# Kernel tuning notes

Hardware: AMD Instinct MI355X
Metric: run time of the kernel (lower is better)

## Reference

```python
import jax, jax.numpy as jnp
import numpy as np

DIM = 96; HEADS = 3; DHEAD = 32; GSS = 4; PATCH = 32; B = 128; G = 8
INNER = HEADS * DHEAD  # == DIM
SCALE = DHEAD ** -0.5
EPS = 1e-5


def _rbf(x):
    # FastKAN RBF basis on grid [-2, 2] with G centers -> (..., G)
    centers = jnp.linspace(-2.0, 2.0, G)
    h = 4.0 / (G - 1)
    return jnp.exp(-(((x[..., None] - centers) / h) ** 2))


def _kan_pointwise(x, wb, ws):
    # Pointwise KAN conv: (b, Cin, *spatial) -> (b, Cout, *spatial)
    # y = W_base @ silu(x) + W_spline @ rbf(x)
    b, cin = x.shape[0], x.shape[1]
    sp = x.shape[2:]
    xs = x.reshape(b, cin, -1)                       # (b, Cin, L)
    y = jnp.einsum('oi,bil->bol', wb, jax.nn.silu(xs))
    y = y + jnp.einsum('oig,bilg->bol', ws, _rbf(xs))
    return y.reshape(b, wb.shape[0], *sp)


def setup_inputs() -> dict:
    key = jax.random.key(0)
    ks = jax.random.split(key, 8)
    inp = {
        'x': jax.random.normal(ks[0], (B, DIM, PATCH, PATCH), jnp.float32),
        'group_tokens': jax.random.normal(ks[1], (DIM,), jnp.float32),
        'qkv_wb': jax.random.normal(ks[2], (3 * DIM, DIM), jnp.float32) * (DIM ** -0.5),
        'qkv_ws': jax.random.normal(ks[3], (3 * DIM, DIM, G), jnp.float32) * 0.02,
        'ln_g': jnp.ones((DHEAD,), jnp.float32),
        'ln_b': jnp.zeros((DHEAD,), jnp.float32),
        'gt_wb': jax.random.normal(ks[4], (2 * INNER, INNER), jnp.float32) * (INNER ** -0.5),
        'gt_ws': jax.random.normal(ks[5], (2 * INNER, INNER, G), jnp.float32) * 0.02,
        'out_wb': jax.random.normal(ks[6], (DIM, INNER), jnp.float32) * (INNER ** -0.5),
        'out_ws': jax.random.normal(ks[7], (DIM, INNER, G), jnp.float32) * 0.02,
    }
    return inp


def reference(x, group_tokens, qkv_wb, qkv_ws, ln_g, ln_b, gt_wb, gt_ws, out_wb, out_ws):
    b, c, H, W = x.shape
    g = GSS
    nx, ny = H // g, W // g
    nw = nx * ny                                    # number of windows
    bp = b * nw
    n = g * g + 1                                   # window tokens incl. group token

    # b c (h g1) (w g2) -> (b h w) c (g1 g2)
    xw = x.reshape(b, c, nx, g, ny, g).transpose(0, 2, 4, 1, 3, 5).reshape(bp, c, g * g)
    tok = jnp.broadcast_to(group_tokens[None, :, None], (bp, c, 1))
    xw = jnp.concatenate([tok, xw], axis=-1)        # (bp, c, n)

    qkv = _kan_pointwise(xw, qkv_wb, qkv_ws)        # (bp, 3c, n)
    q, k, v = jnp.split(qkv, 3, axis=1)

    def split_heads(t):  # b (h d) n -> b h n d
        return t.reshape(bp, HEADS, DHEAD, n).transpose(0, 1, 3, 2)

    q, k, v = map(split_heads, (q, k, v))
    q = q * SCALE
    # channel-attention within window: contract over token axis n
    dots = jnp.einsum('bhni,bhnj->bhij', q, k)      # (bp, h, d, d)
    attn = jax.nn.softmax(dots, axis=-1)
    out = jnp.einsum('bhij,bhnj->bhni', attn, v)    # (bp, h, n, d)

    gt = out[:, :, 0]                               # (bp, h, d) group tokens
    gf = out[:, :, 1:]                              # (bp, h, g*g, d)
    gt = gt.reshape(b, nw, HEADS, DHEAD).transpose(0, 2, 1, 3)            # (b, h, nw, d)
    gf = gf.reshape(b, nw, HEADS, g * g, DHEAD).transpose(0, 2, 1, 3, 4)  # (b, h, nw, gg, d)

    # group_tokens_to_qk: LN(d) -> GELU -> KAN conv over nw (channels h*d -> 2*h*d)
    mu = gt.mean(-1, keepdims=True)
    var = ((gt - mu) ** 2).mean(-1, keepdims=True)
    h_ = (gt - mu) * jax.lax.rsqrt(var + EPS) * ln_g + ln_b
    h_ = jax.nn.gelu(h_, approximate=False)
    hh = h_.transpose(0, 1, 3, 2).reshape(b, HEADS * DHEAD, nw)           # b (h c) n
    qk = _kan_pointwise(hh, gt_wb, gt_ws)                                 # (b, 2*h*d, nw)
    qk = qk.reshape(b, HEADS, 2 * DHEAD, nw).transpose(0, 1, 3, 2)        # (b, h, nw, 2d)
    w_q, w_k = jnp.split(qk, 2, axis=-1)
    w_q = w_q * SCALE
    w_attn = jax.nn.softmax(jnp.einsum('bhid,bhjd->bhij', w_q, w_k), axis=-1)
    agg = jnp.einsum('bhij,bhjwd->bhiwd', w_attn, gf)                     # (b, h, nw, gg, d)

    # b h (x y) (g1 g2) d -> b (h d) (x g1) (y g2)
    fmap = agg.reshape(b, HEADS, nx, ny, g, g, DHEAD)
    fmap = fmap.transpose(0, 1, 6, 2, 4, 3, 5).reshape(b, HEADS * DHEAD, H, W)

    return _kan_pointwise(fmap, out_wb, out_ws)     # (b, dim, H, W)
```

## Files before the change

### kernel.cpp

```cpp
#include <hip/hip_runtime.h>
#include <cstddef>

#define SCALE 0.17677669529663687f
#define EPS 1e-5f

typedef __attribute__((ext_vector_type(8))) __bf16 bf16x8;
typedef __attribute__((ext_vector_type(16))) float f32x16;
typedef __attribute__((ext_vector_type(8))) unsigned short ushort8;

__device__ __forceinline__ unsigned short f2bf(float f) {
    unsigned u = __float_as_uint(f);
    return (unsigned short)((u + 0x7fffu + ((u >> 16) & 1u)) >> 16);
}
__device__ __forceinline__ float bf2f(unsigned short h) {
    return __uint_as_float(((unsigned)h) << 16);
}
__device__ __forceinline__ unsigned cvt_pk_bf16(float a, float b) {
    unsigned r;
    asm("v_cvt_pk_bf16_f32 %0, %1, %2" : "=v"(r) : "v"(a), "v"(b));
    return r;
}

#define MFMA32(a, b, c) __builtin_amdgcn_mfma_f32_32x32x16_bf16(a, b, c, 0, 0, 0)

#define GLD_LDS16(gsrc, ldst) \
    __builtin_amdgcn_global_load_lds((const __attribute__((address_space(1))) void*)(gsrc), \
                                     (__attribute__((address_space(3))) void*)(ldst), 16, 0, 0)

__global__ __launch_bounds__(256)
void prep_frag32(const float* __restrict__ wb, const float* __restrict__ ws,
                 unsigned short* __restrict__ Wf, int MTT)
{
    int idx = blockIdx.x * 256 + threadIdx.x;
    int total = 27 * MTT * 4 * 64;
    if (idx >= total) return;
    int lane = idx & 63;
    int t = idx >> 6;
    int hl = t & 1, kf = (t >> 1) & 1;
    int mt = (t >> 2) % MTT, s = (t >> 2) / MTT;
    int cg = s / 9, f = s - cg * 9;
    int m = mt * 32 + (lane & 31);
    int kg = lane >> 5;
    ushort8 v;
    #pragma unroll
    for (int j = 0; j < 8; ++j) {
        int c = cg * 32 + kf * 16 + kg * 8 + j;
        float w = (f == 0) ? wb[m * 96 + c] : ws[(m * 96 + c) * 8 + (f - 1)];
        unsigned short hi = f2bf(w);
        v[j] = hl ? f2bf(w - bf2f(hi)) : hi;
    }
    *reinterpret_cast<ushort8*>(Wf + (size_t)t * 512 + lane * 8) = v;
}

template<int MTT, int MODE>
__global__ __launch_bounds__(256, 2)
void kan_mfma(const float* __restrict__ xin, const float* __restrict__ token,
              const unsigned short* __restrict__ Wf, float* __restrict__ out)
{
    __shared__ __align__(16) char smem[2 * 12 * 1024];

    const int tid = threadIdx.x, lane = tid & 63, wid = tid >> 6;
    const int kg = lane >> 5, cl = lane & 31;

    int n0, mb;
    if (MODE == 0) {
        int xcd = blockIdx.x & 7, idx = blockIdx.x >> 3;
        int nloc = idx / 3; mb = idx - nloc * 3;
        n0 = (xcd * 68 + nloc) * 256;
    } else {
        mb = blockIdx.x & 1; n0 = (blockIdx.x >> 1) * 256;
    }

    auto issueA = [&](int s, int buf) {
        #pragma unroll
        for (int c0 = 0; c0 < 3; ++c0) {
            int c = wid + c0 * 4;
            const unsigned short* src = Wf + ((size_t)s * MTT * 4 + mb * 12 + c) * 512 + lane * 8;
            GLD_LDS16(src, smem + (buf * 12 + c) * 1024);
        }
    };
    issueA(0, 0);

    const float* gbv[2];
    int gsv[2];
    #pragma unroll
    for (int nt = 0; nt < 2; ++nt) {
        int p = n0 + wid * 64 + nt * 32 + cl;
        if (MODE == 0) {
            int w = p / 17, l = p - w * 17;
            if (l == 0) { gbv[nt] = token; gsv[nt] = 1; }
            else {
                int b = w >> 6, wl = w & 63;
                int wx = wl >> 3, wy = wl & 7;
                int jj = l - 1, gx = jj >> 2, gy = jj & 3;
                gbv[nt] = xin + (size_t)b * 98304 + (wx * 4 + gx) * 32 + wy * 4 + gy;
                gsv[nt] = 1024;
            }
        } else {
            gbv[nt] = xin + (size_t)(p >> 6) * 6144 + (p & 63);
            gsv[nt] = 64;
        }
    }

    f32x16 acc[2][3];
    #pragma unroll
    for (int nt = 0; nt < 2; ++nt)
        #pragma unroll
        for (int mt = 0; mt < 3; ++mt)
            #pragma unroll
            for (int r = 0; r < 16; ++r) acc[nt][mt][r] = 0.f;

    float rr[2][16], du[2][16];
    bf16x8 pk[2][2];

    auto phiInit = [&](int cg) {
        #pragma unroll
        for (int nt = 0; nt < 2; ++nt) {
            float ph[16];
            #pragma unroll
            for (int t = 0; t < 2; ++t)
                #pragma unroll
                for (int j = 0; j < 8; ++j) {
                    int q = t * 8 + j;
                    float xv = gbv[nt][(size_t)(cg * 32 + t * 16 + kg * 8 + j) * gsv[nt]];
                    ph[q] = __fdividef(xv, 1.f + __expf(-xv));
                    float a = fmaf(xv, 1.75f, 3.5f);
                    rr[nt][q] = __expf(-a * a);
                    du[nt][q] = __expf(fminf(fmaf(a, 2.f, -1.f), 80.f));
                }
            #pragma unroll
            for (int t = 0; t < 2; ++t) {
                uint4 w;
                w.x = cvt_pk_bf16(ph[t * 8 + 0], ph[t * 8 + 1]);
                w.y = cvt_pk_bf16(ph[t * 8 + 2], ph[t * 8 + 3]);
                w.z = cvt_pk_bf16(ph[t * 8 + 4], ph[t * 8 + 5]);
                w.w = cvt_pk_bf16(ph[t * 8 + 6], ph[t * 8 + 7]);
                pk[nt][t] = *reinterpret_cast<bf16x8*>(&w);
            }
        }
    };
    auto phiRbf = [&](bool upd) {
        #pragma unroll
        for (int nt = 0; nt < 2; ++nt) {
            if (upd) {
                #pragma unroll
                for (int q = 0; q < 16; ++q) { rr[nt][q] *= du[nt][q]; du[nt][q] *= 0.1353352832366127f; }
            }
            #pragma unroll
            for (int t = 0; t < 2; ++t) {
                uint4 w;
                w.x = cvt_pk_bf16(rr[nt][t * 8 + 0], rr[nt][t * 8 + 1]);
                w.y = cvt_pk_bf16(rr[nt][t * 8 + 2], rr[nt][t * 8 + 3]);
                w.z = cvt_pk_bf16(rr[nt][t * 8 + 4], rr[nt][t * 8 + 5]);
                w.w = cvt_pk_bf16(rr[nt][t * 8 + 6], rr[nt][t * 8 + 7]);
                pk[nt][t] = *reinterpret_cast<bf16x8*>(&w);
            }
        }
    };

    #pragma unroll
    for (int s = 0; s < 27; ++s) {
        __syncthreads();
        if (s + 1 < 27) issueA(s + 1, (s + 1) & 1);
        const int fn = s % 9;
        if (fn == 0) phiInit(s / 9);
        else phiRbf(fn != 1);

        const char* Ab = smem + (s & 1) * 12288;
        #pragma unroll
        for (int mt = 0; mt < 3; ++mt) {
            const char* fb = Ab + mt * 4096 + lane * 16;
            bf16x8 b0h = *reinterpret_cast<const bf16x8*>(fb);
            bf16x8 b0l = *reinterpret_cast<const bf16x8*>(fb + 1024);
            bf16x8 b1h = *reinterpret_cast<const bf16x8*>(fb + 2048);
            bf16x8 b1l = *reinterpret_cast<const bf16x8*>(fb + 3072);
            #pragma unroll
            for (int nt = 0; nt < 2; ++nt) {
                acc[nt][mt] = MFMA32(pk[nt][0], b0h, acc[nt][mt]);
                acc[nt][mt] = MFMA32(pk[nt][0], b0l, acc[nt][mt]);
                acc[nt][mt] = MFMA32(pk[nt][1], b1h, acc[nt][mt]);
                acc[nt][mt] = MFMA32(pk[nt][1], b1l, acc[nt][mt]);
            }
        }
    }

    if (MODE == 0) {
        #pragma unroll
        for (int nt = 0; nt < 2; ++nt)
            #pragma unroll
            for (int r = 0; r < 16; ++r) {
                int p = n0 + wid * 64 + nt * 32 + (r & 3) + 8 * (r >> 2) + 4 * kg;
                int w = p / 17, l = p - w * 17;
                float* dst = out + (size_t)w * 4896 + l * 288 + mb * 96 + cl;
                dst[0]  = acc[nt][0][r];
                dst[32] = acc[nt][1][r];
                dst[64] = acc[nt][2][r];
            }
    } else {
        #pragma unroll
        for (int nt = 0; nt < 2; ++nt)
            #pragma unroll
            for (int r = 0; r < 16; ++r) {
                int p = n0 + wid * 64 + nt * 32 + (r & 3) + 8 * (r >> 2) + 4 * kg;
                float* dst = out + (size_t)p * 192 + mb * 96 + cl;
                dst[0]  = acc[nt][0][r];
                dst[32] = acc[nt][1][r];
                dst[64] = acc[nt][2][r];
            }
    }
}

__global__ __launch_bounds__(256, 4)
void kan_mfma_fmap(const float* __restrict__ xin,
                   const unsigned short* __restrict__ Wf, float* __restrict__ out)
{
    __shared__ __align__(16) char smem[40960];
    char* sA = smem;
    char* sB = smem + 24576;

    const int tid = threadIdx.x, lane = tid & 63, wid = tid >> 6;

    int xcd = blockIdx.x & 7;
    int n0 = (xcd * 128 + (blockIdx.x >> 3)) * 128;

    auto issueA = [&](int s, int buf) {
        #pragma unroll
        for (int c0 = 0; c0 < 3; ++c0) {
            int c = wid + c0 * 4;
            const unsigned short* src = Wf + ((size_t)s * 12 + c) * 512 + lane * 8;
            GLD_LDS16(src, sA + (buf * 12 + c) * 1024);
        }
    };
    issueA(0, 0);

    const int ct = tid & 127, kgp = tid >> 7;
    const int lane_in = kgp * 32 + (ct & 31);
    const int p = n0 + ct;
    const float* gbase = xin + (size_t)(p >> 10) * 98304 + (p & 1023);

    f32x16 acc[3];
    #pragma unroll
    for (int mt = 0; mt < 3; ++mt)
        #pragma unroll
        for (int r = 0; r < 16; ++r) acc[mt][r] = 0.f;

    float rr[16], du[16];

    auto phiInit = [&](int cg, char* d0, char* d1) {
        float ph[16];
        #pragma unroll
        for (int t = 0; t < 2; ++t)
            #pragma unroll
            for (int j = 0; j < 8; ++j) {
                int q = t * 8 + j;
                float xv = gbase[(size_t)(cg * 32 + t * 16 + kgp * 8 + j) * 1024];
                ph[q] = __fdividef(xv, 1.f + __expf(-xv));
                float a = fmaf(xv, 1.75f, 3.5f);
                rr[q] = __expf(-a * a);
                du[q] = __expf(fminf(fmaf(a, 2.f, -1.f), 80.f));
            }
        uint4 w0, w1;
        w0.x = cvt_pk_bf16(ph[0], ph[1]);  w0.y = cvt_pk_bf16(ph[2], ph[3]);
        w0.z = cvt_pk_bf16(ph[4], ph[5]);  w0.w = cvt_pk_bf16(ph[6], ph[7]);
        w1.x = cvt_pk_bf16(ph[8], ph[9]);  w1.y = cvt_pk_bf16(ph[10], ph[11]);
        w1.z = cvt_pk_bf16(ph[12], ph[13]); w1.w = cvt_pk_bf16(ph[14], ph[15]);
        *reinterpret_cast<uint4*>(d0) = w0;
        *reinterpret_cast<uint4*>(d1) = w1;
    };
    auto phiRbf = [&](bool upd, char* d0, char* d1) {
        if (upd) {
            #pragma unroll
            for (int q = 0; q < 16; ++q) { rr[q] *= du[q]; du[q] *= 0.1353352832366127f; }
        }
        uint4 w0, w1;
        w0.x = cvt_pk_bf16(rr[0], rr[1]);  w0.y = cvt_pk_bf16(rr[2], rr[3]);
        w0.z = cvt_pk_bf16(rr[4], rr[5]);  w0.w = cvt_pk_bf16(rr[6], rr[7]);
        w1.x = cvt_pk_bf16(rr[8], rr[9]);  w1.y = cvt_pk_bf16(rr[10], rr[11]);
        w1.z = cvt_pk_bf16(rr[12], rr[13]); w1.w = cvt_pk_bf16(rr[14], rr[15]);
        *reinterpret_cast<uint4*>(d0) = w0;
        *reinterpret_cast<uint4*>(d1) = w1;
    };

    phiInit(0, sB + (ct >> 5) * 1024 + lane_in * 16,
               sB + (4 + (ct >> 5)) * 1024 + lane_in * 16);

    #pragma unroll
    for (int s = 0; s < 27; ++s) {
        int sb = s & 1;
        __syncthreads();
        if (s + 1 < 27) issueA(s + 1, (s + 1) & 1);
        {
            const char* Ab = sA + sb * 12288;
            const char* Bb = sB + sb * 8192;
            bf16x8 b0 = *reinterpret_cast<const bf16x8*>(Bb + wid * 1024 + lane * 16);
            bf16x8 b1 = *reinterpret_cast<const bf16x8*>(Bb + (4 + wid) * 1024 + lane * 16);
            #pragma unroll
            for (int mt = 0; mt < 3; ++mt) {
                const char* fb = Ab + mt * 4096 + lane * 16;
                bf16x8 a0 = *reinterpret_cast<const bf16x8*>(fb);
                bf16x8 a1 = *reinterpret_cast<const bf16x8*>(fb + 1024);
                bf16x8 a2 = *reinterpret_cast<const bf16x8*>(fb + 2048);
                bf16x8 a3 = *reinterpret_cast<const bf16x8*>(fb + 3072);
                acc[mt] = MFMA32(a0, b0, acc[mt]);
                acc[mt] = MFMA32(a1, b0, acc[mt]);
                acc[mt] = MFMA32(a2, b1, acc[mt]);
                acc[mt] = MFMA32(a3, b1, acc[mt]);
            }
        }
        if (s + 1 < 27) {
            char* d0 = sB + ((s + 1) & 1) * 8192 + (ct >> 5) * 1024 + lane_in * 16;
            int fn = (s + 1) % 9;
            if (fn == 0) phiInit((s + 1) / 9, d0, d0 + 4096);
            else phiRbf(fn != 1, d0, d0 + 4096);
        }
    }

    const int colL = n0 + wid * 32 + (lane & 31);
    #pragma unroll
    for (int mt = 0; mt < 3; ++mt) {
        #pragma unroll
        for (int r = 0; r < 16; ++r) {
            int row = mt * 32 + (r & 3) + 8 * (r >> 2) + 4 * (lane >> 5);
            out[(size_t)(colL >> 10) * 98304 + (size_t)row * 1024 + (colL & 1023)] = acc[mt][r];
        }
    }
}

__global__ __launch_bounds__(256)
void attn1(const float* __restrict__ qkv, float* __restrict__ gt, float* __restrict__ gf)
{
    __shared__ float sw[17][288];
    __shared__ float sa[3][32][33];
    const int w = blockIdx.x, tid = threadIdx.x;

    const float4* src = reinterpret_cast<const float4*>(qkv + (size_t)w * 4896);
    float4* dstl = reinterpret_cast<float4*>(&sw[0][0]);
    for (int e = tid; e < 1224; e += 256) dstl[e] = src[e];
    __syncthreads();

    for (int e = tid; e < 3072; e += 256) {
        int h = e >> 10, r = e & 1023, i = r >> 5, j = r & 31;
        float s = 0.f;
        #pragma unroll
        for (int l = 0; l < 17; ++l) s += sw[l][h * 32 + i] * sw[l][96 + h * 32 + j];
        sa[h][i][j] = s * SCALE;
    }
    __syncthreads();
    if (tid < 96) {
        int h = tid >> 5, i = tid & 31;
        float m = -1e30f;
        for (int j = 0; j < 32; ++j) m = fmaxf(m, sa[h][i][j]);
        float sum = 0.f;
        for (int j = 0; j < 32; ++j) { float e_ = __expf(sa[h][i][j] - m); sa[h][i][j] = e_; sum += e_; }
        float inv = 1.f / sum;
        for (int j = 0; j < 32; ++j) sa[h][i][j] *= inv;
    }
    __syncthreads();
    const int b = w >> 6, wl = w & 63;
    for (int e = tid; e < 1632; e += 256) {
        int h = e / 544, r = e - h * 544, l = r >> 5, i = r & 31;
        float s = 0.f;
        #pragma unroll
        for (int j = 0; j < 32; ++j) s += sa[h][i][j] * sw[l][192 + h * 32 + j];
        if (l == 0) gt[(((size_t)b * 3 + h) * 64 + wl) * 32 + i] = s;
        else        gf[((((size_t)b * 3 + h) * 64 + wl) * 16 + (l - 1)) * 32 + i] = s;
    }
}

__global__ __launch_bounds__(256)
void ln_gelu(const float* __restrict__ gt, const float* __restrict__ lng,
             const float* __restrict__ lnb, float* __restrict__ hh)
{
    int row = blockIdx.x * 8 + (threadIdx.x >> 5);
    int d = threadIdx.x & 31;
    float x = gt[(size_t)row * 32 + d];
    float s = x, s2 = x * x;
    #pragma unroll
    for (int m = 16; m >= 1; m >>= 1) { s += __shfl_xor(s, m, 32); s2 += __shfl_xor(s2, m, 32); }
    float mu = s * (1.f / 32.f);
    float var = s2 * (1.f / 32.f) - mu * mu;
    float h = (x - mu) * rsqrtf(var + EPS) * lng[d] + lnb[d];
    float g = 0.5f * h * (1.f + erff(h * 0.70710678118654752f));
    int b = row / 192, r = row - b * 192;
    int hd = r >> 6, wl = r & 63;
    hh[((size_t)b * 96 + hd * 32 + d) * 64 + wl] = g;
}

__global__ __launch_bounds__(256)
void attn2a(const float* __restrict__ qk, float* __restrict__ wattn)
{
    int bh = blockIdx.x;
    int b = bh / 3, h = bh - b * 3;
    __shared__ float swq[64][33];
    __shared__ float swk[64][33];
    __shared__ float sd[64][65];
    int tid = threadIdx.x;
    for (int e = tid; e < 2048; e += 256) {
        int i = e >> 5, d = e & 31;
        const float* row = qk + ((size_t)b * 64 + i) * 192 + h * 64;
        swq[i][d] = row[d] * SCALE;
        swk[i][d] = row[32 + d];
    }
    __syncthreads();
    for (int e = tid; e < 4096; e += 256) {
        int i = e >> 6, j = e & 63;
        float s = 0.f;
        #pragma unroll
        for (int d = 0; d < 32; ++d) s += swq[i][d] * swk[j][d];
        sd[i][j] = s;
    }
    __syncthreads();
    if (tid < 64) {
        float m = -1e30f;
        for (int j = 0; j < 64; ++j) m = fmaxf(m, sd[tid][j]);
        float sum = 0.f;
        for (int j = 0; j < 64; ++j) { float e_ = __expf(sd[tid][j] - m); sd[tid][j] = e_; sum += e_; }
        float inv = 1.f / sum;
        for (int j = 0; j < 64; ++j) sd[tid][j] *= inv;
    }
    __syncthreads();
    for (int e = tid; e < 4096; e += 256)
        wattn[(size_t)bh * 4096 + e] = sd[e >> 6][e & 63];
}

__global__ __launch_bounds__(256)
void attn2b(const float* __restrict__ wattn, const float* __restrict__ gf,
            float* __restrict__ fmap)
{
    int blk = blockIdx.x;
    int ct = blk & 3, bh = blk >> 2;
    int b = bh / 3, h = bh - b * 3;
    __shared__ float sa[64][65];
    __shared__ float sg[64][129];
    int tid = threadIdx.x;
    for (int e = tid; e < 4096; e += 256) sa[e >> 6][e & 63] = wattn[(size_t)bh * 4096 + e];
    for (int e = tid; e < 8192; e += 256) {
        int j = e >> 7, c = e & 127;
        sg[j][c] = gf[((size_t)bh * 64 + j) * 512 + ct * 128 + c];
    }
    __syncthreads();
    int txc = tid & 31, tyi = tid >> 5;
    float acc[8][4];
    #pragma unroll
    for (int ii = 0; ii < 8; ++ii)
        #pragma unroll
        for (int c = 0; c < 4; ++c) acc[ii][c] = 0.f;
    for (int j = 0; j < 64; ++j) {
        float g0[4];
        #pragma unroll
        for (int c = 0; c < 4; ++c) g0[c] = sg[j][txc + c * 32];
        #pragma unroll
        for (int ii = 0; ii < 8; ++ii) {
            float a = sa[tyi + ii * 8][j];
            #pragma unroll
            for (int c = 0; c < 4; ++c) acc[ii][c] += a * g0[c];
        }
    }
    __syncthreads();
    #pragma unroll
    for (int ii = 0; ii < 8; ++ii)
        #pragma unroll
        for (int c = 0; c < 4; ++c)
            sg[tyi + ii * 8][txc + c * 32] = acc[ii][c];
    __syncthreads();
    for (int e = tid; e < 8192; e += 256) {
        int d = e >> 8;
        int nx = (e >> 5) & 7;
        int cp = e & 31;
        int ny = cp >> 2, gy = cp & 3;
        float v = sg[nx * 8 + ny][gy * 32 + d];
        fmap[(((size_t)b * 96 + h * 32 + d) * 32 + nx * 4 + ct) * 32 + cp] = v;
    }
}

extern "C" void kernel_launch(void* const* d_in, const int* in_sizes, int n_in,
                              void* d_out, int out_size, void* d_ws, size_t ws_size,
                              hipStream_t stream)
{
    const float* x      = (const float*)d_in[0];
    const float* tok    = (const float*)d_in[1];
    const float* qkv_wb = (const float*)d_in[2];
    const float* qkv_ws = (const float*)d_in[3];
    const float* lng    = (const float*)d_in[4];
    const float* lnb    = (const float*)d_in[5];
    const float* gt_wb  = (const float*)d_in[6];
    const float* gt_ws  = (const float*)d_in[7];
    const float* out_wb = (const float*)d_in[8];
    const float* out_ws = (const float*)d_in[9];
    float* out = (float*)d_out;
    float* ws  = (float*)d_ws;

    const size_t OFF_QKV   = 0;
    const size_t OFF_FMAP  = 0;
    const size_t OFF_WATTN = 12582912;
    const size_t OFF_WF2   = 40108032;
    const size_t OFF_GT    = OFF_WF2 + 165888;
    const size_t OFF_GF    = OFF_GT + 786432;
    const size_t OFF_HH    = OFF_GF + 12582912;
    const size_t OFF_QK    = OFF_HH + 786432;
    const size_t OFF_WF1   = OFF_QK + 1572864;
    const size_t OFF_WF3   = OFF_WF1 + 248832;
    const size_t TOTAL     = OFF_WF3 + 82944;
    if (ws_size < TOTAL * sizeof(float)) return;

    unsigned short* wf1 = (unsigned short*)(ws + OFF_WF1);
    unsigned short* wf2 = (unsigned short*)(ws + OFF_WF2);
    unsigned short* wf3 = (unsigned short*)(ws + OFF_WF3);

    prep_frag32<<<243, 256, 0, stream>>>(qkv_wb, qkv_ws, wf1, 9);
    prep_frag32<<<162, 256, 0, stream>>>(gt_wb,  gt_ws,  wf2, 6);
    prep_frag32<<< 81, 256, 0, stream>>>(out_wb, out_ws, wf3, 3);

    kan_mfma<9, 0><<<1632, 256, 0, stream>>>(x, tok, wf1, ws + OFF_QKV);
    attn1<<<8192, 256, 0, stream>>>(ws + OFF_QKV, ws + OFF_GT, ws + OFF_GF);
    ln_gelu<<<3072, 256, 0, stream>>>(ws + OFF_GT, lng, lnb, ws + OFF_HH);
    kan_mfma<6, 2><<<64, 256, 0, stream>>>(ws + OFF_HH, nullptr, wf2, ws + OFF_QK);
    attn2a<<<384, 256, 0, stream>>>(ws + OFF_QK, ws + OFF_WATTN);
    attn2b<<<1536, 256, 0, stream>>>(ws + OFF_WATTN, ws + OFF_GF, ws + OFF_FMAP);
    kan_mfma_fmap<<<1024, 256, 0, stream>>>(ws + OFF_FMAP, wf3, out);
}
```

Baseline: 461.2 us.

## Quad-buffer weight fragments in KAN MFMA and fuse LN-GELU into attn1

```diff
diff --git a/kernel.cpp b/kernel.cpp
--- a/kernel.cpp
+++ b/kernel.cpp
@@ -57,7 +57,7 @@
 void kan_mfma(const float* __restrict__ xin, const float* __restrict__ token,
               const unsigned short* __restrict__ Wf, float* __restrict__ out)
 {
-    __shared__ __align__(16) char smem[2 * 12 * 1024];
+    __shared__ __align__(16) char smem[4 * 12 * 1024];
 
     const int tid = threadIdx.x, lane = tid & 63, wid = tid >> 6;
     const int kg = lane >> 5, cl = lane & 31;
@@ -80,6 +80,7 @@
         }
     };
     issueA(0, 0);
+    issueA(1, 1);
 
     const float* gbv[2];
     int gsv[2];
@@ -158,31 +159,40 @@
         }
     };
 
-    #pragma unroll
-    for (int s = 0; s < 27; ++s) {
-        __syncthreads();
-        if (s + 1 < 27) issueA(s + 1, (s + 1) & 1);
-        const int fn = s % 9;
-        if (fn == 0) phiInit(s / 9);
-        else phiRbf(fn != 1);
-
-        const char* Ab = smem + (s & 1) * 12288;
-        #pragma unroll
-        for (int mt = 0; mt < 3; ++mt) {
-            const char* fb = Ab + mt * 4096 + lane * 16;
-            bf16x8 b0h = *reinterpret_cast<const bf16x8*>(fb);
-            bf16x8 b0l = *reinterpret_cast<const bf16x8*>(fb + 1024);
-            bf16x8 b1h = *reinterpret_cast<const bf16x8*>(fb + 2048);
-            bf16x8 b1l = *reinterpret_cast<const bf16x8*>(fb + 3072);
-            #pragma unroll
-            for (int nt = 0; nt < 2; ++nt) {
-                acc[nt][mt] = MFMA32(pk[nt][0], b0h, acc[nt][mt]);
-                acc[nt][mt] = MFMA32(pk[nt][0], b0l, acc[nt][mt]);
-                acc[nt][mt] = MFMA32(pk[nt][1], b1h, acc[nt][mt]);
-                acc[nt][mt] = MFMA32(pk[nt][1], b1l, acc[nt][mt]);
-            }
-        }
-    }
+#define KSTEP(S) {                                                              \
+        if ((S) % 9 == 0) phiInit((S) / 9);                                     \
+        else phiRbf(((S) % 9) != 1);                                            \
+        const char* Ab = smem + ((S) & 3) * 12288;                              \
+        _Pragma("unroll")                                                       \
+        for (int mt = 0; mt < 3; ++mt) {                                        \
+            const char* fb = Ab + mt * 4096 + lane * 16;                        \
+            bf16x8 b0h = *reinterpret_cast<const bf16x8*>(fb);                  \
+            bf16x8 b0l = *reinterpret_cast<const bf16x8*>(fb + 1024);           \
+            bf16x8 b1h = *reinterpret_cast<const bf16x8*>(fb + 2048);           \
+            bf16x8 b1l = *reinterpret_cast<const bf16x8*>(fb + 3072);           \
+            _Pragma("unroll")                                                   \
+            for (int nt = 0; nt < 2; ++nt) {                                    \
+                acc[nt][mt] = MFMA32(pk[nt][0], b0h, acc[nt][mt]);              \
+                acc[nt][mt] = MFMA32(pk[nt][0], b0l, acc[nt][mt]);              \
+                acc[nt][mt] = MFMA32(pk[nt][1], b1h, acc[nt][mt]);              \
+                acc[nt][mt] = MFMA32(pk[nt][1], b1l, acc[nt][mt]);              \
+            }                                                                   \
+        }                                                                       \
+    }
+#define SUPER(S) {                                                              \
+        __syncthreads();                                                        \
+        if ((S) + 2 < 27) issueA((S) + 2, ((S) + 2) & 3);                       \
+        if ((S) + 3 < 27) issueA((S) + 3, ((S) + 3) & 3);                       \
+        KSTEP(S)                                                                \
+        KSTEP((S) + 1)                                                          \
+    }
+
+    SUPER(0)  SUPER(2)  SUPER(4)  SUPER(6)  SUPER(8)  SUPER(10) SUPER(12)
+    SUPER(14) SUPER(16) SUPER(18) SUPER(20) SUPER(22) SUPER(24)
+    __syncthreads();
+    KSTEP(26)
+#undef SUPER
+#undef KSTEP
 
     if (MODE == 0) {
         #pragma unroll
@@ -327,10 +337,13 @@
 }
 
 __global__ __launch_bounds__(256)
-void attn1(const float* __restrict__ qkv, float* __restrict__ gt, float* __restrict__ gf)
+void attn1(const float* __restrict__ qkv, const float* __restrict__ lng,
+           const float* __restrict__ lnb, float* __restrict__ gf,
+           float* __restrict__ hh)
 {
     __shared__ float sw[17][288];
     __shared__ float sa[3][32][33];
+    __shared__ float sgt[3][32];
     const int w = blockIdx.x, tid = threadIdx.x;
 
     const float4* src = reinterpret_cast<const float4*>(qkv + (size_t)w * 4896);
@@ -362,28 +375,22 @@
         float s = 0.f;
         #pragma unroll
         for (int j = 0; j < 32; ++j) s += sa[h][i][j] * sw[l][192 + h * 32 + j];
-        if (l == 0) gt[(((size_t)b * 3 + h) * 64 + wl) * 32 + i] = s;
+        if (l == 0) sgt[h][i] = s;
         else        gf[((((size_t)b * 3 + h) * 64 + wl) * 16 + (l - 1)) * 32 + i] = s;
     }
-}
-
-__global__ __launch_bounds__(256)
-void ln_gelu(const float* __restrict__ gt, const float* __restrict__ lng,
-             const float* __restrict__ lnb, float* __restrict__ hh)
-{
-    int row = blockIdx.x * 8 + (threadIdx.x >> 5);
-    int d = threadIdx.x & 31;
-    float x = gt[(size_t)row * 32 + d];
-    float s = x, s2 = x * x;
-    #pragma unroll
-    for (int m = 16; m >= 1; m >>= 1) { s += __shfl_xor(s, m, 32); s2 += __shfl_xor(s2, m, 32); }
-    float mu = s * (1.f / 32.f);
-    float var = s2 * (1.f / 32.f) - mu * mu;
-    float h = (x - mu) * rsqrtf(var + EPS) * lng[d] + lnb[d];
-    float g = 0.5f * h * (1.f + erff(h * 0.70710678118654752f));
-    int b = row / 192, r = row - b * 192;
-    int hd = r >> 6, wl = r & 63;
-    hh[((size_t)b * 96 + hd * 32 + d) * 64 + wl] = g;
+    __syncthreads();
+    if (tid < 96) {
+        int h = tid >> 5, d = tid & 31;
+        float xv = sgt[h][d];
+        float s1 = xv, s2 = xv * xv;
+        #pragma unroll
+        for (int m = 16; m >= 1; m >>= 1) { s1 += __shfl_xor(s1, m, 32); s2 += __shfl_xor(s2, m, 32); }
+        float mu = s1 * (1.f / 32.f);
+        float var = s2 * (1.f / 32.f) - mu * mu;
+        float hv = (xv - mu) * rsqrtf(var + EPS) * lng[d] + lnb[d];
+        float g = 0.5f * hv * (1.f + erff(hv * 0.70710678118654752f));
+        hh[((size_t)b * 96 + h * 32 + d) * 64 + wl] = g;
+    }
 }
 
 __global__ __launch_bounds__(256)
@@ -512,8 +519,7 @@
     prep_frag32<<< 81, 256, 0, stream>>>(out_wb, out_ws, wf3, 3);
 
     kan_mfma<9, 0><<<1632, 256, 0, stream>>>(x, tok, wf1, ws + OFF_QKV);
-    attn1<<<8192, 256, 0, stream>>>(ws + OFF_QKV, ws + OFF_GT, ws + OFF_GF);
-    ln_gelu<<<3072, 256, 0, stream>>>(ws + OFF_GT, lng, lnb, ws + OFF_HH);
+    attn1<<<8192, 256, 0, stream>>>(ws + OFF_QKV, lng, lnb, ws + OFF_GF, ws + OFF_HH);
     kan_mfma<6, 2><<<64, 256, 0, stream>>>(ws + OFF_HH, nullptr, wf2, ws + OFF_QK);
     attn2a<<<384, 256, 0, stream>>>(ws + OFF_QK, ws + OFF_WATTN);
     attn2b<<<1536, 256, 0, stream>>>(ws + OFF_WATTN, ws + OFF_GF, ws + OFF_FMAP);
```

Measured after the change: 441.9 us. -4.2%, faster.
